# Kernel tuning notes

Hardware: AMD Instinct MI355X
Metric: run time of the kernel (lower is better)

Reference implementation:

```python
import jax, jax.numpy as jnp
import numpy as np

B, T, D, K = 16, 1024, 256, 1024
DECAY = 0.99
EPS = 1e-5


def setup_inputs() -> dict:
    key = jax.random.key(0)
    k1, k2 = jax.random.split(key)
    x = jax.random.normal(k1, (B, T, D), dtype=jnp.float32)
    # nn.Embedding weight initialized uniform(-1/num_emb, 1/num_emb)
    embed_w = jax.random.uniform(k2, (K, D), dtype=jnp.float32,
                                 minval=-1.0 / K, maxval=1.0 / K)
    ema_cluster_size = jnp.zeros((K,), dtype=jnp.float32)
    ema_w = embed_w  # self._ema_w = embed.weight.clone()
    return {"x": x, "embed_w": embed_w,
            "ema_cluster_size": ema_cluster_size, "ema_w": ema_w}


def reference(x, embed_w, ema_cluster_size, ema_w):
    input_shape = x.shape
    flat = x.reshape(-1, input_shape[-1])          # [N, D]
    N = flat.shape[0]

    dist = (jnp.sum(flat * flat, axis=1, keepdims=True)
            + jnp.sum(embed_w * embed_w, axis=1)[None, :]
            - 2.0 * jnp.matmul(flat, embed_w.T))
    idx = jnp.argmin(dist, axis=-1)                # [N] int32

    # one_hot @ W  ==  gather rows of codebook
    quant_flat = embed_w[idx]                      # [N, D]
    # straight-through estimator (custom backward passes grad to input only)
    quant_flat = flat + jax.lax.stop_gradient(quant_flat - flat)
    quantized = quant_flat.reshape(input_shape)

    # ---- training-mode EMA updates (enc_idx.sum(0) == counts; enc_idx.T @ flat == segment_sum) ----
    counts = jax.ops.segment_sum(jnp.ones((N,), dtype=flat.dtype), idx,
                                 num_segments=K)
    cs = ema_cluster_size * DECAY + (1.0 - DECAY) * counts
    n = jnp.sum(cs)
    cs = (cs + EPS) / (n + K * EPS) * n
    dw = jax.ops.segment_sum(flat, idx, num_segments=K)   # [K, D]
    ema_w_new = ema_w * DECAY + (1.0 - DECAY) * dw
    embed_new = ema_w_new / cs[:, None]

    # commitment loss (quantized detached)
    e_latent_loss = jnp.mean((x - jax.lax.stop_gradient(quantized)) ** 2)
    loss = 0.25 * e_latent_loss

    return quantized, loss, embed_new, cs, ema_w_new
```

## Files before the change

### kernel.cpp

```cpp
#include <hip/hip_runtime.h>
#include <cstdint>
#include <cstddef>

namespace {
constexpr int NROW = 16384;
constexpr int KC   = 1024;
constexpr int DIM  = 256;
constexpr int MT   = 128;
constexpr int KSPLIT = 8;
constexpr int KPB  = KC / KSPLIT;
constexpr int FCAP = 8192;
constexpr int RPB  = 4;
}

typedef __attribute__((ext_vector_type(8))) short bf16x8;
typedef __attribute__((ext_vector_type(4))) float f32x4;
typedef unsigned long long u64;
typedef uint32_t u32;

__device__ __forceinline__ unsigned fkey(float s) {
  unsigned u = __float_as_uint(s);
  return ((int)u >= 0) ? (u ^ 0x80000000u) : ~u;
}
__device__ __forceinline__ float unfkey(unsigned u) {
  return __uint_as_float((u & 0x80000000u) ? (u ^ 0x80000000u) : ~u);
}

__device__ __forceinline__ void split2(float a, u32& h, u32& l) {
  const u32 u  = __float_as_uint(a);
  const u32 rh = (u + 0x7fffu + ((u >> 16) & 1u)) >> 16;
  const float ah = __uint_as_float(rh << 16);
  const float al = a - ah;
  const u32 v  = __float_as_uint(al);
  const u32 rl = (v + 0x7fffu + ((v >> 16) & 1u)) >> 16;
  h = rh & 0xffffu; l = rl & 0xffffu;
}

__device__ __forceinline__ float np_sumsq_256(const float* __restrict__ p) {
  float half[2];
  #pragma unroll
  for (int h = 0; h < 2; h++) {
    const float* q = p + h * 128;
    float r[8];
    #pragma unroll
    for (int j = 0; j < 8; j++) r[j] = __fmul_rn(q[j], q[j]);
    #pragma unroll 1
    for (int i = 8; i < 128; i += 8)
      #pragma unroll
      for (int j = 0; j < 8; j++)
        r[j] = __fadd_rn(r[j], __fmul_rn(q[i + j], q[i + j]));
    half[h] = __fadd_rn(__fadd_rn(__fadd_rn(r[0], r[1]), __fadd_rn(r[2], r[3])),
                        __fadd_rn(__fadd_rn(r[4], r[5]), __fadd_rn(r[6], r[7])));
  }
  return __fadd_rn(half[0], half[1]);
}

__global__ __launch_bounds__(256)
void pack_wnorm_kernel(const float4* __restrict__ x4, const float4* __restrict__ w4,
                       const float* __restrict__ w,
                       uint4* __restrict__ xh4, uint4* __restrict__ xl4,
                       uint4* __restrict__ wh4, uint4* __restrict__ wl4,
                       float* __restrict__ wnorm) {
  if (blockIdx.x >= 2176) {
    const int k = (blockIdx.x - 2176) * 256 + threadIdx.x;
    wnorm[k] = np_sumsq_256(&w[k * DIM]);
    return;
  }
  const int g = blockIdx.x * 256 + threadIdx.x;
  const float4* src; uint4* dh; uint4* dl; int gg;
  if (g < 524288) { gg = g;          src = x4; dh = xh4; dl = xl4; }
  else            { gg = g - 524288; src = w4; dh = wh4; dl = wl4; }
  const float4 a = src[gg * 2], b = src[gg * 2 + 1];
  u32 h[8], l[8];
  split2(a.x, h[0], l[0]); split2(a.y, h[1], l[1]);
  split2(a.z, h[2], l[2]); split2(a.w, h[3], l[3]);
  split2(b.x, h[4], l[4]); split2(b.y, h[5], l[5]);
  split2(b.z, h[6], l[6]); split2(b.w, h[7], l[7]);
  uint4 H, L;
  H.x = h[0] | (h[1] << 16); H.y = h[2] | (h[3] << 16);
  H.z = h[4] | (h[5] << 16); H.w = h[6] | (h[7] << 16);
  L.x = l[0] | (l[1] << 16); L.y = l[2] | (l[3] << 16);
  L.z = l[4] | (l[5] << 16); L.w = l[6] | (l[7] << 16);
  dh[gg] = H; dl[gg] = L;
}

__global__ __launch_bounds__(256, 4)
void dist_mfma_kernel(const ushort* __restrict__ xh, const ushort* __restrict__ xl,
                      const ushort* __restrict__ wh, const ushort* __restrict__ wl,
                      const float* __restrict__ wnorm,
                      u64* __restrict__ pairs) {
  __shared__ __align__(16) u32 lds[8192];

  const int tid  = threadIdx.x;
  const int lane = tid & 63;
  const int wv   = tid >> 6;
  const int quad = lane >> 4;
  const int idx16 = lane & 15;
  const int bid  = blockIdx.x;
  const int rowBase = (((bid >> 6) << 3) | (bid & 7)) * MT;
  const int sp      = (bid >> 3) & 7;
  const int kbase   = sp * KPB;

  const int subrow = lane >> 2, grp = lane & 3;
  const int sgrp = grp ^ ((subrow >> 1) & 3);
  const ushort* gptr[8];
  u32 ldst[8];
  #pragma unroll
  for (int j = 0; j < 8; j++) {
    const int c = wv * 8 + j;
    const ushort* plane; int r0; u32 dstB;
    if (c < 8)       { plane = xh + rowBase * DIM; r0 = c * 16;        dstB = c * 1024; }
    else if (c < 16) { plane = xl + rowBase * DIM; r0 = (c - 8) * 16;  dstB = 8192 + (c - 8) * 1024; }
    else if (c < 24) { plane = wh + kbase * DIM;   r0 = (c - 16) * 16; dstB = 16384 + (c - 16) * 1024; }
    else             { plane = wl + kbase * DIM;   r0 = (c - 24) * 16; dstB = 24576 + (c - 24) * 1024; }
    gptr[j] = plane + (r0 + subrow) * DIM + sgrp * 8;
    ldst[j] = dstB >> 2;
  }

  f32x4 acc[2][8];
  #pragma unroll
  for (int rt = 0; rt < 2; rt++)
    #pragma unroll
    for (int ct = 0; ct < 8; ct++) acc[rt][ct] = (f32x4){0.f, 0.f, 0.f, 0.f};

  const int slotOff = (quad ^ ((idx16 >> 1) & 3)) * 16;

  #pragma unroll 1
  for (int kc = 0; kc < DIM / 32; kc++) {
    __syncthreads();
    #pragma unroll
    for (int j = 0; j < 8; j++) {
      __builtin_amdgcn_global_load_lds(
          (const __attribute__((address_space(1))) u32*)(gptr[j]),
          (__attribute__((address_space(3))) u32*)&lds[ldst[j]], 16, 0, 0);
      gptr[j] += 32;
    }
    __syncthreads();

    bf16x8 Ah[2], Al[2];
    #pragma unroll
    for (int rt = 0; rt < 2; rt++) {
      const int ar = wv * 32 + rt * 16 + idx16;
      Ah[rt] = *(const bf16x8*)((const char*)lds + ar * 64 + slotOff);
      Al[rt] = *(const bf16x8*)((const char*)lds + 8192 + ar * 64 + slotOff);
    }
    #pragma unroll
    for (int ct = 0; ct < 8; ct++) {
      const int br = ct * 16 + idx16;
      const bf16x8 Bh = *(const bf16x8*)((const char*)lds + 16384 + br * 64 + slotOff);
      const bf16x8 Bl = *(const bf16x8*)((const char*)lds + 24576 + br * 64 + slotOff);
      #pragma unroll
      for (int rt = 0; rt < 2; rt++) {
        acc[rt][ct] = __builtin_amdgcn_mfma_f32_16x16x32_bf16(Al[rt], Bh, acc[rt][ct], 0, 0, 0);
        acc[rt][ct] = __builtin_amdgcn_mfma_f32_16x16x32_bf16(Ah[rt], Bl, acc[rt][ct], 0, 0, 0);
        acc[rt][ct] = __builtin_amdgcn_mfma_f32_16x16x32_bf16(Ah[rt], Bh, acc[rt][ct], 0, 0, 0);
      }
    }
  }

  u64 b0[2][4], b1[2][4];
  #pragma unroll
  for (int rt = 0; rt < 2; rt++)
    #pragma unroll
    for (int reg = 0; reg < 4; reg++) { b0[rt][reg] = ~0ULL; b1[rt][reg] = ~0ULL; }

  #pragma unroll
  for (int ct = 0; ct < 8; ct++) {
    const int col = kbase + ct * 16 + idx16;
    const float wn = wnorm[col];
    #pragma unroll
    for (int rt = 0; rt < 2; rt++) {
      #pragma unroll
      for (int reg = 0; reg < 4; reg++) {
        const float s = fmaf(-2.0f, acc[rt][ct][reg], wn);
        const u64 p = ((u64)fkey(s) << 32) | (unsigned)col;
        if (p < b1[rt][reg]) {
          if (p < b0[rt][reg]) { b1[rt][reg] = b0[rt][reg]; b0[rt][reg] = p; }
          else                 { b1[rt][reg] = p; }
        }
      }
    }
  }

  #pragma unroll
  for (int m = 1; m <= 8; m <<= 1) {
    #pragma unroll
    for (int rt = 0; rt < 2; rt++) {
      #pragma unroll
      for (int reg = 0; reg < 4; reg++) {
        const u64 o0 = __shfl_xor(b0[rt][reg], m);
        const u64 o1 = __shfl_xor(b1[rt][reg], m);
        if (o0 < b0[rt][reg]) {
          b1[rt][reg] = (b0[rt][reg] < o1) ? b0[rt][reg] : o1;
          b0[rt][reg] = o0;
        } else {
          b1[rt][reg] = (b1[rt][reg] < o0) ? b1[rt][reg] : o0;
        }
      }
    }
  }

  if (idx16 == 0) {
    #pragma unroll
    for (int rt = 0; rt < 2; rt++) {
      #pragma unroll
      for (int reg = 0; reg < 4; reg++) {
        const int row = rowBase + wv * 32 + rt * 16 + quad * 4 + reg;
        pairs[row * 16 + sp * 2 + 0] = b0[rt][reg];
        pairs[row * 16 + sp * 2 + 1] = b1[rt][reg];
      }
    }
  }
}

__global__ __launch_bounds__(256)
void merge_kernel(const u64* __restrict__ pairs,
                  int* __restrict__ idx, float* __restrict__ counts,
                  int* __restrict__ flags, int* __restrict__ counter) {
  const int row = blockIdx.x * 256 + threadIdx.x;
  const u64* p = &pairs[row * 16];
  u64 B0 = p[0], B1 = p[1];
  #pragma unroll
  for (int s = 1; s < KSPLIT; s++) {
    const u64 c0 = p[s * 2], c1 = p[s * 2 + 1];
    if (c0 < B0) { B1 = (B0 < c1) ? B0 : c1; B0 = c0; }
    else         { B1 = (B1 < c0) ? B1 : c0; }
  }
  const int k = (int)(B0 & 0xffffffffULL);
  idx[row] = k;
  atomicAdd(&counts[k], 1.0f);
  const float s0 = unfkey((unsigned)(B0 >> 32));
  const float s1 = unfkey((unsigned)(B1 >> 32));
  if (s1 - s0 < 2e-4f) {
    const int pos = atomicAdd(counter, 1);
    if (pos < FCAP) flags[pos] = row;
  }
}

__global__ __launch_bounds__(1024)
void recheck_np_kernel(const float* __restrict__ x, const float* __restrict__ w,
                       const float* __restrict__ wnorm,
                       const int* __restrict__ flags, const int* __restrict__ counter,
                       int* __restrict__ idx, float* __restrict__ counts) {
  __shared__ float  xs[RPB][DIM];
  __shared__ double xd[RPB][DIM];
  __shared__ float  x2sh[RPB];
  __shared__ u64    red[RPB][16];

  const int cnt  = min(*counter, FCAP);
  const int base = blockIdx.x * RPB;
  if (base >= cnt) return;
  const int nr = min(RPB, cnt - base);

  {
    const int r = threadIdx.x >> 8, d = threadIdx.x & 255;
    const float v = (r < nr) ? x[flags[base + r] * DIM + d] : 0.0f;
    xs[r][d] = v;
    xd[r][d] = (double)v;
  }
  __syncthreads();
  if (threadIdx.x < RPB) x2sh[threadIdx.x] = np_sumsq_256(xs[threadIdx.x]);
  __syncthreads();

  double x2d[RPB];
  #pragma unroll
  for (int r = 0; r < RPB; r++) x2d[r] = (double)x2sh[r];

  const int k = threadIdx.x;
  const float* __restrict__ wr = &w[k * DIM];
  const double w2 = (double)wnorm[k];

  double dot[RPB];
  #pragma unroll
  for (int r = 0; r < RPB; r++) dot[r] = 0.0;

  float4 wv[4];
  #pragma unroll
  for (int q = 0; q < 4; q++) wv[q] = *(const float4*)&wr[q * 4];

  #pragma unroll 1
  for (int d = 0; d < DIM; d += 16) {
    float4 cur[4];
    #pragma unroll
    for (int q = 0; q < 4; q++) cur[q] = wv[q];
    if (d + 16 < DIM) {
      #pragma unroll
      for (int q = 0; q < 4; q++) wv[q] = *(const float4*)&wr[d + 16 + q * 4];
    }
    #pragma unroll
    for (int q = 0; q < 4; q++) {
      const double wa = (double)cur[q].x, wb = (double)cur[q].y,
                   wc = (double)cur[q].z, wd_ = (double)cur[q].w;
      #pragma unroll
      for (int r = 0; r < RPB; r++) {
        dot[r] = fma(xd[r][d + q * 4 + 0], wa,  dot[r]);
        dot[r] = fma(xd[r][d + q * 4 + 1], wb,  dot[r]);
        dot[r] = fma(xd[r][d + q * 4 + 2], wc,  dot[r]);
        dot[r] = fma(xd[r][d + q * 4 + 3], wd_, dot[r]);
      }
    }
  }

  u64 key[RPB];
  #pragma unroll
  for (int r = 0; r < RPB; r++) {
    const float mmf = (float)dot[r];
    const float S1  = (float)(x2d[r] + w2);
    const float D   = (float)((double)S1 - 2.0 * (double)mmf);
    key[r] = ((u64)fkey(D) << 32) | (unsigned)k;
  }

  #pragma unroll
  for (int m = 1; m < 64; m <<= 1) {
    #pragma unroll
    for (int r = 0; r < RPB; r++) {
      const u64 o = __shfl_xor(key[r], m);
      if (o < key[r]) key[r] = o;
    }
  }
  if ((threadIdx.x & 63) == 0) {
    const int wid = threadIdx.x >> 6;
    #pragma unroll
    for (int r = 0; r < RPB; r++) red[r][wid] = key[r];
  }
  __syncthreads();
  if (threadIdx.x < 64) {
    const int r = threadIdx.x >> 4, l = threadIdx.x & 15;
    u64 kk = red[r][l];
    #pragma unroll
    for (int m = 1; m < 16; m <<= 1) {
      const u64 o = __shfl_xor(kk, m);
      if (o < kk) kk = o;
    }
    if (l == 0 && r < nr) {
      const int row  = flags[base + r];
      const int newk = (int)(kk & 0xffffffffULL);
      const int oldk = idx[row];
      if (newk != oldk) {
        idx[row] = newk;
        atomicAdd(&counts[newk],  1.0f);
        atomicAdd(&counts[oldk], -1.0f);
      }
    }
  }
}

__global__ __launch_bounds__(1024)
void prefix_cs_kernel(const float* __restrict__ ema_cs, const float* __restrict__ counts,
                      int* __restrict__ starts, int* __restrict__ cursor,
                      float* __restrict__ out_cs, float* __restrict__ cs_ws) {
  __shared__ int sc[1024];
  __shared__ float lds[17];
  const int t = threadIdx.x;
  const int ci = (int)counts[t];
  sc[t] = ci;
  const float c = ema_cs[t] * 0.99f + 0.01f * counts[t];
  float v = c;
  #pragma unroll
  for (int off = 32; off > 0; off >>= 1) v += __shfl_down(v, off);
  if ((t & 63) == 0) lds[t >> 6] = v;
  __syncthreads();
  if (t == 0) {
    float n = 0.0f;
    for (int i = 0; i < 16; i++) n += lds[i];
    lds[16] = n;
  }
  __syncthreads();
  const float n = lds[16];
  const float csv = (c + 1e-5f) / (n + 1024.0f * 1e-5f) * n;
  out_cs[t] = csv;
  cs_ws[t]  = csv;
  #pragma unroll
  for (int off = 1; off < 1024; off <<= 1) {
    const int add = (t >= off) ? sc[t - off] : 0;
    __syncthreads();
    sc[t] += add;
    __syncthreads();
  }
  const int excl = sc[t] - ci;
  starts[t] = excl;
  cursor[t] = excl;
}

__global__ __launch_bounds__(256)
void scatter_kernel(const int* __restrict__ idx, int* __restrict__ cursor,
                    int* __restrict__ bucket) {
  const int row = blockIdx.x * 256 + threadIdx.x;
  const int k = idx[row];
  const int pos = atomicAdd(&cursor[k], 1);
  bucket[pos] = row;
}

__global__ __launch_bounds__(256)
void dw_bucket_kernel(const float4* __restrict__ x4, const int* __restrict__ bucket,
                      const int* __restrict__ starts, const float* __restrict__ counts,
                      float4* __restrict__ dw4) {
  __shared__ float4 red[4][64];
  const int k   = blockIdx.x;
  const int d4  = threadIdx.x & 63;
  const int rg  = threadIdx.x >> 6;
  const int s   = starts[k];
  const int e   = s + (int)counts[k];
  float4 acc = {0.f, 0.f, 0.f, 0.f};
  for (int i = s + rg; i < e; i += 4) {
    const float4 v = x4[bucket[i] * 64 + d4];
    acc.x += v.x; acc.y += v.y; acc.z += v.z; acc.w += v.w;
  }
  red[rg][d4] = acc;
  __syncthreads();
  if (rg == 0) {
    const float4 a1 = red[1][d4], a2 = red[2][d4], a3 = red[3][d4];
    acc.x += a1.x + a2.x + a3.x;
    acc.y += a1.y + a2.y + a3.y;
    acc.z += a1.z + a2.z + a3.z;
    acc.w += a1.w + a2.w + a3.w;
    dw4[k * 64 + d4] = acc;
  }
}

__global__ __launch_bounds__(256)
void quant_loss_kernel(const float4* __restrict__ x4,
                       const float4* __restrict__ w4,
                       const int* __restrict__ idx,
                       float4* __restrict__ outq,
                       float* __restrict__ partials) {
  __shared__ float lds[4];
  const int g  = blockIdx.x * 256 + threadIdx.x;
  const int n  = g >> 6;
  const int d4 = g & 63;
  const float4 xv = x4[g];
  const int   k  = idx[n];
  const float4 qv = w4[k * 64 + d4];
  float4 r;
  r.x = xv.x + (qv.x - xv.x);
  r.y = xv.y + (qv.y - xv.y);
  r.z = xv.z + (qv.z - xv.z);
  r.w = xv.w + (qv.w - xv.w);
  outq[g] = r;

  const float dx = xv.x - r.x, dy = xv.y - r.y, dz = xv.z - r.z, dwv = xv.w - r.w;
  float s = dx * dx + dy * dy + dz * dz + dwv * dwv;
  #pragma unroll
  for (int off = 32; off > 0; off >>= 1) s += __shfl_down(s, off);
  if ((threadIdx.x & 63) == 0) lds[threadIdx.x >> 6] = s;
  __syncthreads();
  if (threadIdx.x == 0) partials[blockIdx.x] = lds[0] + lds[1] + lds[2] + lds[3];
}

__global__ __launch_bounds__(256)
void emb_loss_kernel(const float* __restrict__ ema_w, const float* __restrict__ dw,
                     const float* __restrict__ cs, const float* __restrict__ partials,
                     float* __restrict__ out_ema_w, float* __restrict__ out_embed,
                     float* __restrict__ out_loss) {
  if (blockIdx.x == 1024) {
    __shared__ float lds[4];
    float s = 0.0f;
    for (int i = threadIdx.x; i < 4096; i += 256) s += partials[i];
    #pragma unroll
    for (int off = 32; off > 0; off >>= 1) s += __shfl_down(s, off);
    if ((threadIdx.x & 63) == 0) lds[threadIdx.x >> 6] = s;
    __syncthreads();
    if (threadIdx.x == 0) {
      const float total = lds[0] + lds[1] + lds[2] + lds[3];
      out_loss[0] = 0.25f * (total / 4194304.0f);
    }
    return;
  }
  const int g = blockIdx.x * 256 + threadIdx.x;
  const int k = g >> 8;
  const float e = ema_w[g] * 0.99f + 0.01f * dw[g];
  out_ema_w[g] = e;
  out_embed[g] = e / cs[k];
}

extern "C" void kernel_launch(void* const* d_in, const int* in_sizes, int n_in,
                              void* d_out, int out_size, void* d_ws, size_t ws_size,
                              hipStream_t stream) {
  const float* x       = (const float*)d_in[0];
  const float* embed_w = (const float*)d_in[1];
  const float* ema_cs  = (const float*)d_in[2];
  const float* ema_w   = (const float*)d_in[3];

  float* out        = (float*)d_out;
  float* out_q      = out;
  float* out_loss   = out + 4194304;
  float* out_embed  = out + 4194305;
  float* out_cs     = out + 4456449;
  float* out_ema_w  = out + 4457473;

  char* ws = (char*)d_ws;
  u64*   pairs    = (u64*)  (ws + 0);
  int*   bucket   = (int*)  (ws + 0);
  float* dw       = (float*)(ws + 1048576);
  int*   idx      = (int*)  (ws + 2097152);
  float* counts   = (float*)(ws + 2162688);
  int*   counter  = (int*)  (ws + 2166784);
  int*   flags    = (int*)  (ws + 2166912);
  float* wnorm    = (float*)(ws + 2199680);
  float* cs_ws    = (float*)(ws + 2203776);
  float* partials = (float*)(ws + 2207872);
  int*   starts   = (int*)  (ws + 2224256);
  int*   cursor   = (int*)  (ws + 2228352);
  ushort* wh      = (ushort*)(ws + 2232448);
  ushort* wl      = (ushort*)(ws + 2756736);

  ushort* xh = (ushort*)out_q;
  ushort* xl = (ushort*)out_q + 4194304;

  hipMemsetAsync(counts, 0, 4100, stream);

  pack_wnorm_kernel<<<2180, 256, 0, stream>>>(
      (const float4*)x, (const float4*)embed_w, embed_w,
      (uint4*)xh, (uint4*)xl, (uint4*)wh, (uint4*)wl, wnorm);
  dist_mfma_kernel<<<(NROW / MT) * KSPLIT, 256, 0, stream>>>(xh, xl, wh, wl, wnorm, pairs);
  merge_kernel<<<NROW / 256, 256, 0, stream>>>(pairs, idx, counts, flags, counter);
  recheck_np_kernel<<<FCAP / RPB, 1024, 0, stream>>>(x, embed_w, wnorm, flags, counter,
                                                     idx, counts);
  prefix_cs_kernel<<<1, 1024, 0, stream>>>(ema_cs, counts, starts, cursor, out_cs, cs_ws);
  scatter_kernel<<<NROW / 256, 256, 0, stream>>>(idx, cursor, bucket);
  dw_bucket_kernel<<<KC, 256, 0, stream>>>((const float4*)x, bucket, starts, counts,
                                           (float4*)dw);
  quant_loss_kernel<<<NROW * 64 / 256, 256, 0, stream>>>(
      (const float4*)x, (const float4*)embed_w, idx, (float4*)out_q, partials);
  emb_loss_kernel<<<KC * DIM / 256 + 1, 256, 0, stream>>>(
      ema_w, dw, cs_ws, partials, out_ema_w, out_embed, out_loss);
}
```

Before: 194.8 us.

## Fuse dw segment-sum into quant kernel via float atomics, drop bucket sort

```diff
diff --git a/kernel.cpp b/kernel.cpp
--- a/kernel.cpp
+++ b/kernel.cpp
@@ -241,11 +241,14 @@
 void recheck_np_kernel(const float* __restrict__ x, const float* __restrict__ w,
                        const float* __restrict__ wnorm,
                        const int* __restrict__ flags, const int* __restrict__ counter,
-                       int* __restrict__ idx, float* __restrict__ counts) {
+                       int* __restrict__ idx, float* __restrict__ counts,
+                       float* __restrict__ dwz) {
   __shared__ float  xs[RPB][DIM];
   __shared__ double xd[RPB][DIM];
   __shared__ float  x2sh[RPB];
   __shared__ u64    red[RPB][16];
+
+  if (blockIdx.x < 256) dwz[blockIdx.x * 1024 + threadIdx.x] = 0.0f;
 
   const int cnt  = min(*counter, FCAP);
   const int base = blockIdx.x * RPB;
@@ -347,13 +350,9 @@
 
 __global__ __launch_bounds__(1024)
 void prefix_cs_kernel(const float* __restrict__ ema_cs, const float* __restrict__ counts,
-                      int* __restrict__ starts, int* __restrict__ cursor,
                       float* __restrict__ out_cs, float* __restrict__ cs_ws) {
-  __shared__ int sc[1024];
   __shared__ float lds[17];
   const int t = threadIdx.x;
-  const int ci = (int)counts[t];
-  sc[t] = ci;
   const float c = ema_cs[t] * 0.99f + 0.01f * counts[t];
   float v = c;
   #pragma unroll
@@ -370,52 +369,6 @@
   const float csv = (c + 1e-5f) / (n + 1024.0f * 1e-5f) * n;
   out_cs[t] = csv;
   cs_ws[t]  = csv;
-  #pragma unroll
-  for (int off = 1; off < 1024; off <<= 1) {
-    const int add = (t >= off) ? sc[t - off] : 0;
-    __syncthreads();
-    sc[t] += add;
-    __syncthreads();
-  }
-  const int excl = sc[t] - ci;
-  starts[t] = excl;
-  cursor[t] = excl;
-}
-
-__global__ __launch_bounds__(256)
-void scatter_kernel(const int* __restrict__ idx, int* __restrict__ cursor,
-                    int* __restrict__ bucket) {
-  const int row = blockIdx.x * 256 + threadIdx.x;
-  const int k = idx[row];
-  const int pos = atomicAdd(&cursor[k], 1);
-  bucket[pos] = row;
-}
-
-__global__ __launch_bounds__(256)
-void dw_bucket_kernel(const float4* __restrict__ x4, const int* __restrict__ bucket,
-                      const int* __restrict__ starts, const float* __restrict__ counts,
-                      float4* __restrict__ dw4) {
-  __shared__ float4 red[4][64];
-  const int k   = blockIdx.x;
-  const int d4  = threadIdx.x & 63;
-  const int rg  = threadIdx.x >> 6;
-  const int s   = starts[k];
-  const int e   = s + (int)counts[k];
-  float4 acc = {0.f, 0.f, 0.f, 0.f};
-  for (int i = s + rg; i < e; i += 4) {
-    const float4 v = x4[bucket[i] * 64 + d4];
-    acc.x += v.x; acc.y += v.y; acc.z += v.z; acc.w += v.w;
-  }
-  red[rg][d4] = acc;
-  __syncthreads();
-  if (rg == 0) {
-    const float4 a1 = red[1][d4], a2 = red[2][d4], a3 = red[3][d4];
-    acc.x += a1.x + a2.x + a3.x;
-    acc.y += a1.y + a2.y + a3.y;
-    acc.z += a1.z + a2.z + a3.z;
-    acc.w += a1.w + a2.w + a3.w;
-    dw4[k * 64 + d4] = acc;
-  }
 }
 
 __global__ __launch_bounds__(256)
@@ -423,7 +376,8 @@
                        const float4* __restrict__ w4,
                        const int* __restrict__ idx,
                        float4* __restrict__ outq,
-                       float* __restrict__ partials) {
+                       float* __restrict__ partials,
+                       float* __restrict__ dwp) {
   __shared__ float lds[4];
   const int g  = blockIdx.x * 256 + threadIdx.x;
   const int n  = g >> 6;
@@ -438,6 +392,12 @@
   r.w = xv.w + (qv.w - xv.w);
   outq[g] = r;
 
+  float* dwc = &dwp[(k << 8) + (d4 << 2)];
+  atomicAdd(&dwc[0], xv.x);
+  atomicAdd(&dwc[1], xv.y);
+  atomicAdd(&dwc[2], xv.z);
+  atomicAdd(&dwc[3], xv.w);
+
   const float dx = xv.x - r.x, dy = xv.y - r.y, dz = xv.z - r.z, dwv = xv.w - r.w;
   float s = dx * dx + dy * dy + dz * dz + dwv * dwv;
   #pragma unroll
@@ -490,7 +450,6 @@
 
   char* ws = (char*)d_ws;
   u64*   pairs    = (u64*)  (ws + 0);
-  int*   bucket   = (int*)  (ws + 0);
   float* dw       = (float*)(ws + 1048576);
   int*   idx      = (int*)  (ws + 2097152);
   float* counts   = (float*)(ws + 2162688);
@@ -499,8 +458,6 @@
   float* wnorm    = (float*)(ws + 2199680);
   float* cs_ws    = (float*)(ws + 2203776);
   float* partials = (float*)(ws + 2207872);
-  int*   starts   = (int*)  (ws + 2224256);
-  int*   cursor   = (int*)  (ws + 2228352);
   ushort* wh      = (ushort*)(ws + 2232448);
   ushort* wl      = (ushort*)(ws + 2756736);
 
@@ -515,13 +472,10 @@
   dist_mfma_kernel<<<(NROW / MT) * KSPLIT, 256, 0, stream>>>(xh, xl, wh, wl, wnorm, pairs);
   merge_kernel<<<NROW / 256, 256, 0, stream>>>(pairs, idx, counts, flags, counter);
   recheck_np_kernel<<<FCAP / RPB, 1024, 0, stream>>>(x, embed_w, wnorm, flags, counter,
-                                                     idx, counts);
-  prefix_cs_kernel<<<1, 1024, 0, stream>>>(ema_cs, counts, starts, cursor, out_cs, cs_ws);
-  scatter_kernel<<<NROW / 256, 256, 0, stream>>>(idx, cursor, bucket);
-  dw_bucket_kernel<<<KC, 256, 0, stream>>>((const float4*)x, bucket, starts, counts,
-                                           (float4*)dw);
+                                                     idx, counts, dw);
+  prefix_cs_kernel<<<1, 1024, 0, stream>>>(ema_cs, counts, out_cs, cs_ws);
   quant_loss_kernel<<<NROW * 64 / 256, 256, 0, stream>>>(
-      (const float4*)x, (const float4*)embed_w, idx, (float4*)out_q, partials);
+      (const float4*)x, (const float4*)embed_w, idx, (float4*)out_q, partials, dw);
   emb_loss_kernel<<<KC * DIM / 256 + 1, 256, 0, stream>>>(
       ema_w, dw, cs_ws, partials, out_ema_w, out_embed, out_loss);
 }
```

Measured after the change: 235.1 us. 1.21x slower.
